# Optimization experiments

Hardware: AMD Instinct MI355X
Metric: run time of the kernel (lower is better)

## Reference

```python
import jax, jax.numpy as jnp
import numpy as np

N = 100000
E = 1600000
D = 128
L = 2
NEG_SLOPE = 0.2
LN_EPS = 1e-5


def setup_inputs() -> dict:
    key = jax.random.key(0)
    ks = jax.random.split(key, 12)
    x = jax.random.normal(ks[0], (N, D), dtype=jnp.float32)
    src = jax.random.randint(ks[1], (E,), 0, N)
    dst = jax.random.randint(ks[2], (E,), 0, N)
    dst = jnp.where(src == dst, (dst + 1) % N, dst)  # no pre-existing self-loops
    edge_index = jnp.stack([src, dst]).astype(jnp.int64)
    edge_weight = jax.random.uniform(ks[3], (E,), dtype=jnp.float32)
    s = 1.0 / np.sqrt(D)
    W = jax.random.normal(ks[4], (L, D, D), dtype=jnp.float32) * s
    att_src = jax.random.normal(ks[5], (L, D), dtype=jnp.float32) * s
    att_dst = jax.random.normal(ks[6], (L, D), dtype=jnp.float32) * s
    lin_edge_w = jax.random.normal(ks[7], (L, D), dtype=jnp.float32) * s  # Linear(1, D) weight
    att_edge = jax.random.normal(ks[8], (L, D), dtype=jnp.float32) * s
    bias = jnp.zeros((L, D), dtype=jnp.float32)
    ln_gamma = jnp.ones((D,), dtype=jnp.float32)
    ln_beta = jnp.zeros((D,), dtype=jnp.float32)
    return {"x": x, "edge_index": edge_index, "edge_weight": edge_weight,
            "W": W, "att_src": att_src, "att_dst": att_dst,
            "lin_edge_w": lin_edge_w, "att_edge": att_edge, "bias": bias,
            "ln_gamma": ln_gamma, "ln_beta": ln_beta}


def _gat_layer(x, src_f, dst_f, ew_f, W, a_src, a_dst, lew, a_edge, b):
    # x: [N, D]; src_f/dst_f/ew_f already include self-loops -> [E+N]
    h = x @ W                      # [N, D]
    alpha_s = h @ a_src            # [N]
    alpha_d = h @ a_dst            # [N]
    # edge_attr = ew[:,None] * lew; (edge_attr * att_edge).sum(-1) == ew * (lew . att_edge)
    alpha_e = ew_f * jnp.dot(lew, a_edge)           # [E+N]
    logits = jax.nn.leaky_relu(alpha_s[src_f] + alpha_d[dst_f] + alpha_e, NEG_SLOPE)
    # segment softmax over incoming edges of each destination node
    m = jax.ops.segment_max(logits, dst_f, num_segments=N)   # every node has a self-loop
    p = jnp.exp(logits - m[dst_f])
    z = jax.ops.segment_sum(p, dst_f, num_segments=N)
    coef = p / z[dst_f]                                      # [E+N]
    out = jax.ops.segment_sum(h[src_f] * coef[:, None], dst_f, num_segments=N)
    return out + b


def reference(x, edge_index, edge_weight, W, att_src, att_dst, lin_edge_w, att_edge, bias, ln_gamma, ln_beta):
    src, dst = edge_index[0], edge_index[1]
    # add_self_loops with fill_value='mean': loop weight = mean of incoming edge weights
    deg = jax.ops.segment_sum(jnp.ones_like(edge_weight), dst, num_segments=N)
    loop_w = jax.ops.segment_sum(edge_weight, dst, num_segments=N) / jnp.maximum(deg, 1.0)
    ar = jnp.arange(N)
    src_f = jnp.concatenate([src, ar])
    dst_f = jnp.concatenate([dst, ar])
    ew_f = jnp.concatenate([edge_weight, loop_w])
    xx = x
    for l in range(L):
        xx = _gat_layer(xx, src_f, dst_f, ew_f, W[l], att_src[l], att_dst[l],
                        lin_edge_w[l], att_edge[l], bias[l])
        xx = jax.nn.gelu(xx, approximate=False)
    xx = x + xx
    mu = jnp.mean(xx, axis=-1, keepdims=True)
    var = jnp.mean((xx - mu) ** 2, axis=-1, keepdims=True)
    return (xx - mu) * jax.lax.rsqrt(var + LN_EPS) * ln_gamma + ln_beta
```

## Files before the change

### kernel.cpp

```cpp
#include <hip/hip_runtime.h>
#include <hip/hip_bf16.h>
#include <math.h>

#define N_NODES 100000
#define N_EDGES 1600000
#define D 128
#define NEG 0.2f
#define LN_EPS 1e-5f

#define GEMM_BLOCKS ((N_NODES + 63) / 64)
#define PLACE_BLOCKS ((N_EDGES + 1023) / 1024)

typedef __attribute__((ext_vector_type(8))) short bf16x8;
typedef __attribute__((ext_vector_type(4))) float f32x4;

__device__ __forceinline__ float lrelu(float v){ return fmaxf(v, NEG * v); }
__device__ __forceinline__ float gelu_exact(float v){ return 0.5f * v * (1.0f + erff(v * 0.7071067811865476f)); }
__device__ __forceinline__ float wave_sum(float v){
#pragma unroll
  for (int o = 32; o; o >>= 1) v += __shfl_xor(v, o, 64);
  return v;
}
__device__ __forceinline__ unsigned short f2bf(float f){
  __hip_bfloat16 h = __float2bfloat16(f);
  return *(unsigned short*)&h;
}
__device__ __forceinline__ float bf_lo(unsigned u){ return __uint_as_float(u << 16); }
__device__ __forceinline__ float bf_hi(unsigned u){ return __uint_as_float(u & 0xFFFF0000u); }

__global__ __launch_bounds__(256) void k_prep(const float* __restrict__ W,
                                              unsigned short* __restrict__ wfrag,
                                              const float* __restrict__ lew,
                                              const float* __restrict__ ae,
                                              float* __restrict__ c_e){
  if (threadIdx.x < 128){
    int l = threadIdx.x >> 6;
    int lane = threadIdx.x & 63;
    const float* a = lew + l * D;
    const float* b = ae + l * D;
    float v = a[lane] * b[lane] + a[64 + lane] * b[64 + lane];
    v = wave_sum(v);
    if (lane == 0) c_e[l] = v;
  }
#pragma unroll
  for (int it = 0; it < 16; it++){
    int slot = it * 256 + threadIdx.x;
    int lane = slot & 63;
    int kc   = (slot >> 6) & 3;
    int ct   = (slot >> 8) & 7;
    int l    = (slot >> 11) & 1;
    int quad = lane >> 4, n = (lane & 15) + ct * 16;
    const float* Wl = W + l * D * D;
    bf16x8 v;
#pragma unroll
    for (int j = 0; j < 8; j++){
      int k = kc * 32 + quad * 8 + j;
      v[j] = (short)f2bf(Wl[k * D + n]);
    }
    *(bf16x8*)(wfrag + (size_t)slot * 8) = v;
  }
}

template<bool ABF>
__device__ __forceinline__ void gemm_mfma(int gb,
                                          const void* __restrict__ xin_,
                                          const unsigned short* __restrict__ wfrag_l,
                                          const float* __restrict__ att_s,
                                          const float* __restrict__ att_d,
                                          unsigned short* __restrict__ hb,
                                          float* __restrict__ alpha_s,
                                          float* __restrict__ alpha_d){
  __shared__ __align__(16) unsigned short hstage[64 * 136];
  int tid = threadIdx.x;
  int wv = tid >> 6, lane = tid & 63;
  int quad = lane >> 4, c15 = lane & 15;
  int row0 = gb * 64 + wv * 16;

  int arow = min(row0 + c15, N_NODES - 1);
  bf16x8 a[4];
  if constexpr (ABF){
    const unsigned short* xr = (const unsigned short*)xin_ + (size_t)arow * D;
#pragma unroll
    for (int kc = 0; kc < 4; kc++)
      a[kc] = *(const bf16x8*)(xr + kc * 32 + quad * 8);
  } else {
    const float* xr = (const float*)xin_ + (size_t)arow * D;
#pragma unroll
    for (int kc = 0; kc < 4; kc++){
      float4 p = *(const float4*)(xr + kc * 32 + quad * 8);
      float4 q = *(const float4*)(xr + kc * 32 + quad * 8 + 4);
      bf16x8 t;
      t[0] = (short)f2bf(p.x); t[1] = (short)f2bf(p.y);
      t[2] = (short)f2bf(p.z); t[3] = (short)f2bf(p.w);
      t[4] = (short)f2bf(q.x); t[5] = (short)f2bf(q.y);
      t[6] = (short)f2bf(q.z); t[7] = (short)f2bf(q.w);
      a[kc] = t;
    }
  }

  f32x4 acc[8];
#pragma unroll
  for (int ct = 0; ct < 8; ct++) acc[ct] = (f32x4){0.f, 0.f, 0.f, 0.f};

#pragma unroll
  for (int ct = 0; ct < 8; ct++){
#pragma unroll
    for (int kc = 0; kc < 4; kc++){
      bf16x8 b = *(const bf16x8*)(wfrag_l + ((size_t)(ct * 4 + kc) * 64 + lane) * 8);
      acc[ct] = __builtin_amdgcn_mfma_f32_16x16x32_bf16(a[kc], b, acc[ct], 0, 0, 0);
    }
  }

  float attsv[8], attdv[8];
#pragma unroll
  for (int ct = 0; ct < 8; ct++){
    attsv[ct] = att_s[ct * 16 + c15];
    attdv[ct] = att_d[ct * 16 + c15];
  }
#pragma unroll
  for (int reg = 0; reg < 4; reg++){
    float ps = 0.f, pd = 0.f;
#pragma unroll
    for (int ct = 0; ct < 8; ct++){
      ps += acc[ct][reg] * attsv[ct];
      pd += acc[ct][reg] * attdv[ct];
    }
#pragma unroll
    for (int o = 8; o; o >>= 1){
      ps += __shfl_xor(ps, o, 64);
      pd += __shfl_xor(pd, o, 64);
    }
    int row = row0 + quad * 4 + reg;
    if (c15 == reg && row < N_NODES){ alpha_s[row] = ps; alpha_d[row] = pd; }
  }

#pragma unroll
  for (int ct = 0; ct < 8; ct++)
#pragma unroll
    for (int reg = 0; reg < 4; reg++)
      hstage[(wv * 16 + quad * 4 + reg) * 136 + ct * 16 + c15] = f2bf(acc[ct][reg]);
  __syncthreads();
#pragma unroll
  for (int i = 0; i < 4; i++){
    int flat = i * 256 + tid;
    int row = flat >> 4, c = flat & 15;
    int grow = gb * 64 + row;
    if (grow < N_NODES)
      *(uint4*)(hb + (size_t)grow * D + c * 8) = *(const uint4*)(hstage + row * 136 + c * 8);
  }
}

__global__ __launch_bounds__(256, 4) void k_gemm1_place(const float* __restrict__ xin,
                                                        const unsigned short* __restrict__ wfrag,
                                                        const float* __restrict__ att_s,
                                                        const float* __restrict__ att_d,
                                                        unsigned short* __restrict__ hb,
                                                        float* __restrict__ alpha_s,
                                                        float* __restrict__ alpha_d,
                                                        const int* __restrict__ ei,
                                                        const float* __restrict__ ew,
                                                        int* __restrict__ counter,
                                                        int2* __restrict__ csr, int cap){
  if (blockIdx.x >= PLACE_BLOCKS){
    gemm_mfma<false>(blockIdx.x - PLACE_BLOCKS, xin, wfrag, att_s, att_d, hb, alpha_s, alpha_d);
  } else {
    int pb = blockIdx.x;
    int e0 = pb * 1024 + threadIdx.x;
    int ss[4], dd[4], pp[4]; float wwv[4]; bool va[4];
#pragma unroll
    for (int i = 0; i < 4; i++){
      int e = e0 + i * 256;
      va[i] = e < N_EDGES;
      ss[i] = va[i] ? ei[e] : 0;
      dd[i] = va[i] ? ei[N_EDGES + e] : 0;
      wwv[i] = va[i] ? ew[e] : 0.f;
    }
#pragma unroll
    for (int i = 0; i < 4; i++) if (va[i]) pp[i] = atomicAdd(&counter[dd[i]], 1);
#pragma unroll
    for (int i = 0; i < 4; i++)
      if (va[i] && pp[i] < cap)
        csr[(size_t)dd[i] * cap + pp[i]] = make_int2(ss[i], __float_as_int(wwv[i]));
  }
}

__global__ __launch_bounds__(256, 4) void k_gemm_alpha(const unsigned short* __restrict__ xin,
                                                       const unsigned short* __restrict__ wfrag,
                                                       const float* __restrict__ att_s,
                                                       const float* __restrict__ att_d,
                                                       unsigned short* __restrict__ hb,
                                                       float* __restrict__ alpha_s,
                                                       float* __restrict__ alpha_d){
  gemm_mfma<true>(blockIdx.x, xin, wfrag, att_s, att_d, hb, alpha_s, alpha_d);
}

template<bool LN>
__global__ __launch_bounds__(256) void k_agg(const unsigned short* __restrict__ hb,
                                             const float* __restrict__ alpha_s,
                                             const float* __restrict__ alpha_d,
                                             const int* __restrict__ counter,
                                             const int2* __restrict__ csr, int cap,
                                             const float* __restrict__ c_e, int layer,
                                             const float* __restrict__ bias,
                                             const float* __restrict__ xres,
                                             const float* __restrict__ gamma,
                                             const float* __restrict__ beta,
                                             float* __restrict__ outp,
                                             unsigned short* __restrict__ outp_bf){
  int lane = threadIdx.x & 63;
  int cg = lane & 15;
  int qbase = lane & 48;
  int n = blockIdx.x * 16 + (threadIdx.x >> 4);
  float c = c_e[layer];
  int deg = counter[n];
  int dg = min(deg, cap);
  size_t rs = (size_t)n * cap;
  float ad = alpha_d[n];
  float as_n = alpha_s[n];

  uint4 u_self = *((const uint4*)(hb + (size_t)n * D) + cg);
  const float* bptr = bias + layer * D + cg * 8;
  float4 b_lo = *(const float4*)(bptr);
  float4 b_hi = *(const float4*)(bptr + 4);
  float4 xr_lo, xr_hi, g_lo, g_hi, bt_lo, bt_hi;
  if constexpr (LN){
    const float* xr = xres + (size_t)n * D + cg * 8;
    xr_lo = *(const float4*)(xr);
    xr_hi = *(const float4*)(xr + 4);
    g_lo  = *(const float4*)(gamma + cg * 8);
    g_hi  = *(const float4*)(gamma + cg * 8 + 4);
    bt_lo = *(const float4*)(beta + cg * 8);
    bt_hi = *(const float4*)(beta + cg * 8 + 4);
  }

  float z = 0.f, wsum = 0.f;
  float acc[8];
#pragma unroll
  for (int k = 0; k < 8; k++) acc[k] = 0.f;

  for (int base = 0; base < dg; base += 16){
    int j = base + cg;
    float p = 0.f; int s = n;
    if (j < dg){
      int2 eg = csr[rs + j];
      s = eg.x;
      float w = __int_as_float(eg.y);
      wsum += w;
      p = __expf(lrelu(alpha_s[s] + ad + c * w));
    }
    z += p;
#pragma unroll
    for (int i = 0; i < 16; i++){
      float pi = __shfl(p, qbase + i, 64);
      int   si = __shfl(s, qbase + i, 64);
      uint4 u = *((const uint4*)(hb + (size_t)si * D) + cg);
      acc[0] += pi * bf_lo(u.x); acc[1] += pi * bf_hi(u.x);
      acc[2] += pi * bf_lo(u.y); acc[3] += pi * bf_hi(u.y);
      acc[4] += pi * bf_lo(u.z); acc[5] += pi * bf_hi(u.z);
      acc[6] += pi * bf_lo(u.w); acc[7] += pi * bf_hi(u.w);
    }
  }
#pragma unroll
  for (int o = 8; o; o >>= 1){
    z += __shfl_xor(z, o, 64);
    wsum += __shfl_xor(wsum, o, 64);
  }

  float lw = wsum / fmaxf((float)deg, 1.0f);
  float ps = __expf(lrelu(as_n + ad + c * lw));
  z += ps;
  acc[0] += ps * bf_lo(u_self.x); acc[1] += ps * bf_hi(u_self.x);
  acc[2] += ps * bf_lo(u_self.y); acc[3] += ps * bf_hi(u_self.y);
  acc[4] += ps * bf_lo(u_self.z); acc[5] += ps * bf_hi(u_self.z);
  acc[6] += ps * bf_lo(u_self.w); acc[7] += ps * bf_hi(u_self.w);

  float inv = 1.0f / z;
  float bv[8] = {b_lo.x, b_lo.y, b_lo.z, b_lo.w, b_hi.x, b_hi.y, b_hi.z, b_hi.w};
  float o[8];
#pragma unroll
  for (int k = 0; k < 8; k++) o[k] = gelu_exact(acc[k] * inv + bv[k]);

  if constexpr (LN){
    float xrv[8] = {xr_lo.x, xr_lo.y, xr_lo.z, xr_lo.w, xr_hi.x, xr_hi.y, xr_hi.z, xr_hi.w};
    float s1 = 0.f;
#pragma unroll
    for (int k = 0; k < 8; k++){ o[k] += xrv[k]; s1 += o[k]; }
#pragma unroll
    for (int ofs = 8; ofs; ofs >>= 1) s1 += __shfl_xor(s1, ofs, 64);
    float mu = s1 * (1.0f / D);
    float s2 = 0.f;
#pragma unroll
    for (int k = 0; k < 8; k++){ o[k] -= mu; s2 += o[k] * o[k]; }
#pragma unroll
    for (int ofs = 8; ofs; ofs >>= 1) s2 += __shfl_xor(s2, ofs, 64);
    float rinv = rsqrtf(s2 * (1.0f / D) + LN_EPS);
    float gv[8] = {g_lo.x, g_lo.y, g_lo.z, g_lo.w, g_hi.x, g_hi.y, g_hi.z, g_hi.w};
    float btv[8] = {bt_lo.x, bt_lo.y, bt_lo.z, bt_lo.w, bt_hi.x, bt_hi.y, bt_hi.z, bt_hi.w};
#pragma unroll
    for (int k = 0; k < 8; k++) o[k] = o[k] * rinv * gv[k] + btv[k];
    float* orow = outp + (size_t)n * D + cg * 8;
    *(float4*)(orow)     = make_float4(o[0], o[1], o[2], o[3]);
    *(float4*)(orow + 4) = make_float4(o[4], o[5], o[6], o[7]);
  } else {
    unsigned short ob[8];
#pragma unroll
    for (int k = 0; k < 8; k++) ob[k] = f2bf(o[k]);
    *(uint4*)(outp_bf + (size_t)n * D + cg * 8) = *(const uint4*)ob;
  }
}

extern "C" void kernel_launch(void* const* d_in, const int* in_sizes, int n_in,
                              void* d_out, int out_size, void* d_ws, size_t ws_size,
                              hipStream_t stream) {
  const float* x     = (const float*)d_in[0];
  const int*   ei    = (const int*)d_in[1];
  const float* ew    = (const float*)d_in[2];
  const float* W     = (const float*)d_in[3];
  const float* att_s = (const float*)d_in[4];
  const float* att_d = (const float*)d_in[5];
  const float* lew   = (const float*)d_in[6];
  const float* ae    = (const float*)d_in[7];
  const float* bias  = (const float*)d_in[8];
  const float* gamma = (const float*)d_in[9];
  const float* beta  = (const float*)d_in[10];
  float* out = (float*)d_out;

  const int N = N_NODES;

  size_t fixed = (size_t)(3 * N + 16) * 4 + 65536;
  size_t need64 = fixed + (size_t)N * 64 * 8 + (size_t)N * D * 2;
  int cap = (ws_size >= need64) ? 64 : 48;

  int*   counter  = (int*)d_ws;
  float* alpha_s  = (float*)(counter + N);
  float* alpha_d  = alpha_s + N;
  float* c_e      = alpha_d + N;
  unsigned short* wfrag = (unsigned short*)(c_e + 16);
  int2*  csr      = (int2*)(wfrag + 32768);
  unsigned short* hb = (unsigned short*)(csr + (size_t)N * cap);

  unsigned short* h1b = (unsigned short*)d_out;

  hipMemsetAsync(counter, 0, (size_t)N * sizeof(int), stream);
  k_prep<<<1, 256, 0, stream>>>(W, wfrag, lew, ae, c_e);

  k_gemm1_place<<<GEMM_BLOCKS + PLACE_BLOCKS, 256, 0, stream>>>(
      x, wfrag, att_s, att_d, hb, alpha_s, alpha_d, ei, ew, counter, csr, cap);

  k_agg<false><<<N / 16, 256, 0, stream>>>(hb, alpha_s, alpha_d, counter, csr, cap,
                                           c_e, 0, bias, nullptr, nullptr, nullptr,
                                           nullptr, h1b);

  k_gemm_alpha<<<GEMM_BLOCKS, 256, 0, stream>>>(h1b, wfrag + 16384, att_s + D, att_d + D,
                                                hb, alpha_s, alpha_d);
  k_agg<true><<<N / 16, 256, 0, stream>>>(hb, alpha_s, alpha_d, counter, csr, cap,
                                          c_e, 1, bias, x, gamma, beta, out, nullptr);
}
```

Measured before the change: 432.3 us.

## Fuse layer-2 GEMM and attention projections into layer-1 aggregation kernel

```diff
diff --git a/kernel.cpp b/kernel.cpp
--- a/kernel.cpp
+++ b/kernel.cpp
@@ -10,6 +10,7 @@
 
 #define GEMM_BLOCKS ((N_NODES + 63) / 64)
 #define PLACE_BLOCKS ((N_EDGES + 1023) / 1024)
+#define AGG_BLOCKS (N_NODES / 16)
 
 typedef __attribute__((ext_vector_type(8))) short bf16x8;
 typedef __attribute__((ext_vector_type(4))) float f32x4;
@@ -171,16 +172,21 @@
     for (int i = 0; i < 4; i++){
       int e = e0 + i * 256;
       va[i] = e < N_EDGES;
-      ss[i] = va[i] ? ei[e] : 0;
-      dd[i] = va[i] ? ei[N_EDGES + e] : 0;
-      wwv[i] = va[i] ? ew[e] : 0.f;
+      int ec = va[i] ? e : 0;
+      ss[i] = __builtin_nontemporal_load(ei + ec);
+      dd[i] = __builtin_nontemporal_load(ei + N_EDGES + ec);
+      wwv[i] = __builtin_nontemporal_load(ew + ec);
     }
 #pragma unroll
     for (int i = 0; i < 4; i++) if (va[i]) pp[i] = atomicAdd(&counter[dd[i]], 1);
 #pragma unroll
     for (int i = 0; i < 4; i++)
-      if (va[i] && pp[i] < cap)
-        csr[(size_t)dd[i] * cap + pp[i]] = make_int2(ss[i], __float_as_int(wwv[i]));
+      if (va[i] && pp[i] < cap){
+        unsigned long long packed =
+            ((unsigned long long)(unsigned)__float_as_int(wwv[i]) << 32) | (unsigned)ss[i];
+        __builtin_nontemporal_store(packed,
+            (unsigned long long*)(csr + (size_t)dd[i] * cap + pp[i]));
+      }
   }
 }
 
@@ -195,23 +201,18 @@
 }
 
 template<bool LN>
-__global__ __launch_bounds__(256) void k_agg(const unsigned short* __restrict__ hb,
-                                             const float* __restrict__ alpha_s,
-                                             const float* __restrict__ alpha_d,
-                                             const int* __restrict__ counter,
-                                             const int2* __restrict__ csr, int cap,
-                                             const float* __restrict__ c_e, int layer,
-                                             const float* __restrict__ bias,
-                                             const float* __restrict__ xres,
-                                             const float* __restrict__ gamma,
-                                             const float* __restrict__ beta,
-                                             float* __restrict__ outp,
-                                             unsigned short* __restrict__ outp_bf){
-  int lane = threadIdx.x & 63;
-  int cg = lane & 15;
-  int qbase = lane & 48;
-  int n = blockIdx.x * 16 + (threadIdx.x >> 4);
-  float c = c_e[layer];
+__device__ __forceinline__ void agg_core(const unsigned short* __restrict__ hb,
+                                         const float* __restrict__ alpha_s,
+                                         const float* __restrict__ alpha_d,
+                                         const int* __restrict__ counter,
+                                         const int2* __restrict__ csr, int cap,
+                                         float c,
+                                         const float* __restrict__ bias_l,
+                                         const float* __restrict__ xres,
+                                         const float* __restrict__ gamma,
+                                         const float* __restrict__ beta,
+                                         int n, int cg, int qbase,
+                                         float o[8]){
   int deg = counter[n];
   int dg = min(deg, cap);
   size_t rs = (size_t)n * cap;
@@ -219,9 +220,8 @@
   float as_n = alpha_s[n];
 
   uint4 u_self = *((const uint4*)(hb + (size_t)n * D) + cg);
-  const float* bptr = bias + layer * D + cg * 8;
-  float4 b_lo = *(const float4*)(bptr);
-  float4 b_hi = *(const float4*)(bptr + 4);
+  float4 b_lo = *(const float4*)(bias_l + cg * 8);
+  float4 b_hi = *(const float4*)(bias_l + cg * 8 + 4);
   float4 xr_lo, xr_hi, g_lo, g_hi, bt_lo, bt_hi;
   if constexpr (LN){
     const float* xr = xres + (size_t)n * D + cg * 8;
@@ -242,9 +242,10 @@
     int j = base + cg;
     float p = 0.f; int s = n;
     if (j < dg){
-      int2 eg = csr[rs + j];
-      s = eg.x;
-      float w = __int_as_float(eg.y);
+      unsigned long long v = __builtin_nontemporal_load(
+          (const unsigned long long*)(csr + rs + j));
+      s = (int)(unsigned)(v & 0xFFFFFFFFull);
+      float w = __int_as_float((int)(v >> 32));
       wsum += w;
       p = __expf(lrelu(alpha_s[s] + ad + c * w));
     }
@@ -261,9 +262,9 @@
     }
   }
 #pragma unroll
-  for (int o = 8; o; o >>= 1){
-    z += __shfl_xor(z, o, 64);
-    wsum += __shfl_xor(wsum, o, 64);
+  for (int ofs = 8; ofs; ofs >>= 1){
+    z += __shfl_xor(z, ofs, 64);
+    wsum += __shfl_xor(wsum, ofs, 64);
   }
 
   float lw = wsum / fmaxf((float)deg, 1.0f);
@@ -276,7 +277,6 @@
 
   float inv = 1.0f / z;
   float bv[8] = {b_lo.x, b_lo.y, b_lo.z, b_lo.w, b_hi.x, b_hi.y, b_hi.z, b_hi.w};
-  float o[8];
 #pragma unroll
   for (int k = 0; k < 8; k++) o[k] = gelu_exact(acc[k] * inv + bv[k]);
 
@@ -298,15 +298,144 @@
     float btv[8] = {bt_lo.x, bt_lo.y, bt_lo.z, bt_lo.w, bt_hi.x, bt_hi.y, bt_hi.z, bt_hi.w};
 #pragma unroll
     for (int k = 0; k < 8; k++) o[k] = o[k] * rinv * gv[k] + btv[k];
-    float* orow = outp + (size_t)n * D + cg * 8;
-    *(float4*)(orow)     = make_float4(o[0], o[1], o[2], o[3]);
-    *(float4*)(orow + 4) = make_float4(o[4], o[5], o[6], o[7]);
-  } else {
-    unsigned short ob[8];
-#pragma unroll
-    for (int k = 0; k < 8; k++) ob[k] = f2bf(o[k]);
-    *(uint4*)(outp_bf + (size_t)n * D + cg * 8) = *(const uint4*)ob;
-  }
+  }
+}
+
+__global__ __launch_bounds__(256) void k_agg1_fused(const unsigned short* __restrict__ hb,
+                                                    const float* __restrict__ alpha_s,
+                                                    const float* __restrict__ alpha_d,
+                                                    const int* __restrict__ counter,
+                                                    const int2* __restrict__ csr, int cap,
+                                                    const float* __restrict__ c_e,
+                                                    const float* __restrict__ bias,
+                                                    const unsigned short* __restrict__ wfrag2,
+                                                    const float* __restrict__ att_s2,
+                                                    const float* __restrict__ att_d2,
+                                                    unsigned short* __restrict__ hb2,
+                                                    float* __restrict__ alpha2_s,
+                                                    float* __restrict__ alpha2_d){
+  __shared__ __align__(16) unsigned short astage[16 * 136];
+  __shared__ float apart_s[16], apart_d[16];
+  int tid = threadIdx.x;
+  int lane = tid & 63;
+  int cg = lane & 15;
+  int qbase = lane & 48;
+  int n = blockIdx.x * 16 + (tid >> 4);
+
+  float o[8];
+  agg_core<false>(hb, alpha_s, alpha_d, counter, csr, cap, c_e[0],
+                  bias, nullptr, nullptr, nullptr, n, cg, qbase, o);
+
+  unsigned short ob[8];
+#pragma unroll
+  for (int k = 0; k < 8; k++) ob[k] = f2bf(o[k]);
+  *(uint4*)(astage + (tid >> 4) * 136 + cg * 8) = *(const uint4*)ob;
+  if (tid < 16){ apart_s[tid] = 0.f; apart_d[tid] = 0.f; }
+  __syncthreads();
+
+  int wv = tid >> 6;
+  int quad = lane >> 4, c15 = lane & 15;
+  bf16x8 a[4];
+#pragma unroll
+  for (int kc = 0; kc < 4; kc++)
+    a[kc] = *(const bf16x8*)(astage + c15 * 136 + kc * 32 + quad * 8);
+
+  f32x4 acc2[2];
+  float attsv[2], attdv[2];
+#pragma unroll
+  for (int t = 0; t < 2; t++){
+    int ct = wv * 2 + t;
+    acc2[t] = (f32x4){0.f, 0.f, 0.f, 0.f};
+#pragma unroll
+    for (int kc = 0; kc < 4; kc++){
+      bf16x8 b = *(const bf16x8*)(wfrag2 + ((size_t)(ct * 4 + kc) * 64 + lane) * 8);
+      acc2[t] = __builtin_amdgcn_mfma_f32_16x16x32_bf16(a[kc], b, acc2[t], 0, 0, 0);
+    }
+    attsv[t] = att_s2[ct * 16 + c15];
+    attdv[t] = att_d2[ct * 16 + c15];
+  }
+
+#pragma unroll
+  for (int reg = 0; reg < 4; reg++){
+    float ps = acc2[0][reg] * attsv[0] + acc2[1][reg] * attsv[1];
+    float pd = acc2[0][reg] * attdv[0] + acc2[1][reg] * attdv[1];
+#pragma unroll
+    for (int ofs = 8; ofs; ofs >>= 1){
+      ps += __shfl_xor(ps, ofs, 64);
+      pd += __shfl_xor(pd, ofs, 64);
+    }
+    if (c15 == reg){
+      atomicAdd(&apart_s[quad * 4 + reg], ps);
+      atomicAdd(&apart_d[quad * 4 + reg], pd);
+    }
+  }
+  __syncthreads();
+
+#pragma unroll
+  for (int t = 0; t < 2; t++){
+    int ct = wv * 2 + t;
+#pragma unroll
+    for (int reg = 0; reg < 4; reg++)
+      astage[(quad * 4 + reg) * 136 + ct * 16 + c15] = f2bf(acc2[t][reg]);
+  }
+  __syncthreads();
+
+  {
+    int row = tid >> 4, ccol = tid & 15;
+    int grow = blockIdx.x * 16 + row;
+    *(uint4*)(hb2 + (size_t)grow * D + ccol * 8) = *(const uint4*)(astage + row * 136 + ccol * 8);
+  }
+  if (tid < 16){
+    int grow = blockIdx.x * 16 + tid;
+    alpha2_s[grow] = apart_s[tid];
+    alpha2_d[grow] = apart_d[tid];
+  }
+}
+
+__global__ __launch_bounds__(256) void k_agg1_plain(const unsigned short* __restrict__ hb,
+                                                    const float* __restrict__ alpha_s,
+                                                    const float* __restrict__ alpha_d,
+                                                    const int* __restrict__ counter,
+                                                    const int2* __restrict__ csr, int cap,
+                                                    const float* __restrict__ c_e,
+                                                    const float* __restrict__ bias,
+                                                    unsigned short* __restrict__ outp_bf){
+  int tid = threadIdx.x;
+  int lane = tid & 63;
+  int cg = lane & 15;
+  int qbase = lane & 48;
+  int n = blockIdx.x * 16 + (tid >> 4);
+  float o[8];
+  agg_core<false>(hb, alpha_s, alpha_d, counter, csr, cap, c_e[0],
+                  bias, nullptr, nullptr, nullptr, n, cg, qbase, o);
+  unsigned short ob[8];
+#pragma unroll
+  for (int k = 0; k < 8; k++) ob[k] = f2bf(o[k]);
+  *(uint4*)(outp_bf + (size_t)n * D + cg * 8) = *(const uint4*)ob;
+}
+
+__global__ __launch_bounds__(256) void k_agg2(const unsigned short* __restrict__ hb,
+                                              const float* __restrict__ alpha_s,
+                                              const float* __restrict__ alpha_d,
+                                              const int* __restrict__ counter,
+                                              const int2* __restrict__ csr, int cap,
+                                              const float* __restrict__ c_e,
+                                              const float* __restrict__ bias,
+                                              const float* __restrict__ xres,
+                                              const float* __restrict__ gamma,
+                                              const float* __restrict__ beta,
+                                              float* __restrict__ outp){
+  int tid = threadIdx.x;
+  int lane = tid & 63;
+  int cg = lane & 15;
+  int qbase = lane & 48;
+  int n = blockIdx.x * 16 + (tid >> 4);
+  float o[8];
+  agg_core<true>(hb, alpha_s, alpha_d, counter, csr, cap, c_e[1],
+                 bias + D, xres, gamma, beta, n, cg, qbase, o);
+  float* orow = outp + (size_t)n * D + cg * 8;
+  *(float4*)(orow)     = make_float4(o[0], o[1], o[2], o[3]);
+  *(float4*)(orow + 4) = make_float4(o[4], o[5], o[6], o[7]);
 }
 
 extern "C" void kernel_launch(void* const* d_in, const int* in_sizes, int n_in,
@@ -327,19 +456,24 @@
 
   const int N = N_NODES;
 
-  size_t fixed = (size_t)(3 * N + 16) * 4 + 65536;
-  size_t need64 = fixed + (size_t)N * 64 * 8 + (size_t)N * D * 2;
-  int cap = (ws_size >= need64) ? 64 : 48;
+  size_t fixed = (size_t)(5 * N + 16) * 4 + 65536;
+  size_t hbB = (size_t)N * D * 2;
+  bool fused; int cap;
+  if      (ws_size >= fixed + (size_t)N * 64 * 8 + 2 * hbB){ fused = true;  cap = 64; }
+  else if (ws_size >= fixed + (size_t)N * 48 * 8 + 2 * hbB){ fused = true;  cap = 48; }
+  else if (ws_size >= fixed + (size_t)N * 64 * 8 + hbB)    { fused = false; cap = 64; }
+  else                                                     { fused = false; cap = 48; }
 
   int*   counter  = (int*)d_ws;
   float* alpha_s  = (float*)(counter + N);
   float* alpha_d  = alpha_s + N;
-  float* c_e      = alpha_d + N;
+  float* alpha2_s = alpha_d + N;
+  float* alpha2_d = alpha2_s + N;
+  float* c_e      = alpha2_d + N;
   unsigned short* wfrag = (unsigned short*)(c_e + 16);
   int2*  csr      = (int2*)(wfrag + 32768);
-  unsigned short* hb = (unsigned short*)(csr + (size_t)N * cap);
-
-  unsigned short* h1b = (unsigned short*)d_out;
+  unsigned short* hb  = (unsigned short*)(csr + (size_t)N * cap);
+  unsigned short* hb2 = hb + (size_t)N * D;
 
   hipMemsetAsync(counter, 0, (size_t)N * sizeof(int), stream);
   k_prep<<<1, 256, 0, stream>>>(W, wfrag, lew, ae, c_e);
@@ -347,12 +481,19 @@
   k_gemm1_place<<<GEMM_BLOCKS + PLACE_BLOCKS, 256, 0, stream>>>(
       x, wfrag, att_s, att_d, hb, alpha_s, alpha_d, ei, ew, counter, csr, cap);
 
-  k_agg<false><<<N / 16, 256, 0, stream>>>(hb, alpha_s, alpha_d, counter, csr, cap,
-                                           c_e, 0, bias, nullptr, nullptr, nullptr,
-                                           nullptr, h1b);
-
-  k_gemm_alpha<<<GEMM_BLOCKS, 256, 0, stream>>>(h1b, wfrag + 16384, att_s + D, att_d + D,
-                                                hb, alpha_s, alpha_d);
-  k_agg<true><<<N / 16, 256, 0, stream>>>(hb, alpha_s, alpha_d, counter, csr, cap,
-                                          c_e, 1, bias, x, gamma, beta, out, nullptr);
-}
+  if (fused){
+    k_agg1_fused<<<AGG_BLOCKS, 256, 0, stream>>>(
+        hb, alpha_s, alpha_d, counter, csr, cap, c_e, bias,
+        wfrag + 16384, att_s + D, att_d + D, hb2, alpha2_s, alpha2_d);
+    k_agg2<<<AGG_BLOCKS, 256, 0, stream>>>(
+        hb2, alpha2_s, alpha2_d, counter, csr, cap, c_e, bias, x, gamma, beta, out);
+  } else {
+    unsigned short* h1b = (unsigned short*)d_out;
+    k_agg1_plain<<<AGG_BLOCKS, 256, 0, stream>>>(
+        hb, alpha_s, alpha_d, counter, csr, cap, c_e, bias, h1b);
+    k_gemm_alpha<<<GEMM_BLOCKS, 256, 0, stream>>>(
+        h1b, wfrag + 16384, att_s + D, att_d + D, hb, alpha_s, alpha_d);
+    k_agg2<<<AGG_BLOCKS, 256, 0, stream>>>(
+        hb, alpha_s, alpha_d, counter, csr, cap, c_e, bias, x, gamma, beta, out);
+  }
+}
```

Result: slower. 474.4 us (+9.7%).
